# Kernel tuning notes

Measured on AMD Instinct MI355X. Metric: run time of the kernel, lower is better.

## Reference

```python
import jax, jax.numpy as jnp
import numpy as np

N = 100000
E = 1600000
F_IN = 128
HID = 64
HEADS = 2
OUT_HEADS = 1
NUM_CLASS = 18
NEG_SLOPE = 0.2


def setup_inputs() -> dict:
    key = jax.random.key(0)
    ks = jax.random.split(key, 12)
    x = jax.random.normal(ks[0], (N, F_IN), dtype=jnp.float32)
    edge_index = jax.random.randint(ks[1], (2, E), 0, N, dtype=jnp.int64)
    s = lambda k, shp, fan: jax.random.normal(k, shp, dtype=jnp.float32) * (1.0 / np.sqrt(fan))
    W0 = s(ks[2], (F_IN, HID), F_IN)
    b0 = jnp.zeros((HID,), dtype=jnp.float32)
    W1 = s(ks[3], (HID, HEADS * HID), HID)
    att_src1 = s(ks[4], (HEADS, HID), HID)
    att_dst1 = s(ks[5], (HEADS, HID), HID)
    b1 = jnp.zeros((HEADS * HID,), dtype=jnp.float32)
    W2 = s(ks[6], (HEADS * HID, OUT_HEADS * NUM_CLASS), HEADS * HID)
    att_src2 = s(ks[7], (OUT_HEADS, NUM_CLASS), NUM_CLASS)
    att_dst2 = s(ks[8], (OUT_HEADS, NUM_CLASS), NUM_CLASS)
    b2 = jnp.zeros((OUT_HEADS * NUM_CLASS,), dtype=jnp.float32)
    return {"x": x, "edge_index": edge_index, "W0": W0, "b0": b0,
            "W1": W1, "att_src1": att_src1, "att_dst1": att_dst1, "b1": b1,
            "W2": W2, "att_src2": att_src2, "att_dst2": att_dst2, "b2": b2}


def gat_conv(x, src, dst, W, att_s, att_d, bias, heads, out_ch):
    n = x.shape[0]
    h = (x @ W).reshape(n, heads, out_ch)              # [N,H,C]
    a_s = jnp.sum(h * att_s, axis=-1)                   # [N,H]
    a_d = jnp.sum(h * att_d, axis=-1)                   # [N,H]
    e = jax.nn.leaky_relu(a_s[src] + a_d[dst], NEG_SLOPE)  # [E,H]
    m = jax.ops.segment_max(e, dst, num_segments=n)
    ex = jnp.exp(e - m[dst])
    denom = jax.ops.segment_sum(ex, dst, num_segments=n)
    alpha = ex / denom[dst]                              # [E,H]
    msg = h[src] * alpha[:, :, None]                     # [E,H,C]
    out = jax.ops.segment_sum(msg, dst, num_segments=n)  # [N,H,C]
    return out.reshape(n, heads * out_ch) + bias


def reference(x, edge_index, W0, b0, W1, att_src1, att_dst1, b1, W2, att_src2, att_dst2, b2):
    n = x.shape[0]
    # PyG GATConv adds self-loops by default
    loops = jnp.arange(n, dtype=edge_index.dtype)
    src = jnp.concatenate([edge_index[0], loops])
    dst = jnp.concatenate([edge_index[1], loops])
    # eval mode: dropout is identity
    h = jax.nn.relu(x @ W0 + b0)
    h = jax.nn.elu(gat_conv(h, src, dst, W1, att_src1, att_dst1, b1, HEADS, HID))
    out = gat_conv(h, src, dst, W2, att_src2, att_dst2, b2, OUT_HEADS, NUM_CLASS)
    return jax.nn.log_softmax(out, axis=-1)
```

## Files before the change

### kernel.cpp

```cpp
#include <hip/hip_runtime.h>
#include <math.h>


#define NEG_SLOPE 0.2f

typedef unsigned short ushort_t;

__device__ __forceinline__ float wmax(float v) {
    for (int o = 32; o; o >>= 1) v = fmaxf(v, __shfl_xor(v, o));
    return v;
}
__device__ __forceinline__ float wsum(float v) {
    for (int o = 32; o; o >>= 1) v += __shfl_xor(v, o);
    return v;
}

__device__ __forceinline__ unsigned bfpack(float a, float b) {
    unsigned ua = __float_as_uint(a);
    unsigned ub = __float_as_uint(b);
    ua = (ua + 0x7fffu + ((ua >> 16) & 1u)) >> 16;
    ub = (ub + 0x7fffu + ((ub >> 16) & 1u)) & 0xffff0000u;
    return ua | ub;
}
__device__ __forceinline__ ushort_t bf16of(float a) {
    unsigned ua = __float_as_uint(a);
    return (ushort_t)((ua + 0x7fffu + ((ua >> 16) & 1u)) >> 16);
}
__device__ __forceinline__ float bflo(unsigned u) { return __uint_as_float(u << 16); }
__device__ __forceinline__ float bfhi(unsigned u) { return __uint_as_float(u & 0xffff0000u); }
__device__ __forceinline__ float bfval(ushort_t u) { return __uint_as_float(((unsigned)u) << 16); }

__global__ void k_deg_init(int* __restrict__ deg, int N) {
    int i = blockIdx.x * blockDim.x + threadIdx.x;
    if (i < N) deg[i] = 1;
}
__global__ void k_deg_edges(const int* __restrict__ ei, int* __restrict__ deg,
                            int* __restrict__ eofs, int E) {
    int e = blockIdx.x * blockDim.x + threadIdx.x;
    if (e < E) eofs[e] = atomicAdd(&deg[ei[E + e]], 1);
}

__global__ __launch_bounds__(256) void k_scan1(const int* __restrict__ deg, int* __restrict__ rs,
                                               int* __restrict__ bsum, int N) {
    __shared__ int s[256];
    int t = threadIdx.x;
    int base = blockIdx.x * 1024;
    int i0 = base + t * 4;
    int d0 = (i0 + 0 < N) ? deg[i0 + 0] : 0;
    int d1 = (i0 + 1 < N) ? deg[i0 + 1] : 0;
    int d2 = (i0 + 2 < N) ? deg[i0 + 2] : 0;
    int d3 = (i0 + 3 < N) ? deg[i0 + 3] : 0;
    int s0 = d0, s1 = s0 + d1, s2 = s1 + d2, s3 = s2 + d3;
    int tsum = s3;
    s[t] = tsum;
    __syncthreads();
    for (int off = 1; off < 256; off <<= 1) {
        int v = (t >= off) ? s[t - off] : 0;
        __syncthreads();
        s[t] += v;
        __syncthreads();
    }
    int excl = s[t] - tsum;
    if (i0 + 0 < N) rs[1 + i0 + 0] = excl + s0;
    if (i0 + 1 < N) rs[1 + i0 + 1] = excl + s1;
    if (i0 + 2 < N) rs[1 + i0 + 2] = excl + s2;
    if (i0 + 3 < N) rs[1 + i0 + 3] = excl + s3;
    if (t == 0) bsum[blockIdx.x] = s[255];
}

__global__ __launch_bounds__(256) void k_scan2(const int* __restrict__ bsum,
                                               int* __restrict__ boff, int NB) {
    __shared__ int s[256];
    int t = threadIdx.x;
    int orig = (t < NB) ? bsum[t] : 0;
    s[t] = orig;
    __syncthreads();
    for (int off = 1; off < 256; off <<= 1) {
        int v = (t >= off) ? s[t - off] : 0;
        __syncthreads();
        s[t] += v;
        __syncthreads();
    }
    if (t < NB) boff[t] = s[t] - orig;
}

__global__ void k_scan3(int* __restrict__ rs, const int* __restrict__ boff, int N) {
    int i = blockIdx.x * blockDim.x + threadIdx.x;
    if (i == 0) rs[0] = 0;
    if (i < N) rs[1 + i] += boff[i >> 10];
}

__global__ __launch_bounds__(256) void k_scatter(const int* __restrict__ ei,
                                                 const int* __restrict__ eofs,
                                                 const int* __restrict__ rs,
                                                 int* __restrict__ csr,
                                                 int E, int Etot, int cohortBlocks) {
    int c = blockIdx.x & 7;
    int pb = blockIdx.x >> 3;
    int tid = pb * 256 + threadIdx.x;
    int stride = cohortBlocks * 256;
    for (int e = tid; e < Etot; e += stride) {
        int dst = (e < E) ? ei[E + e] : (e - E);
        if (((dst >> 13) & 7) != c) continue;
        int src, ofs;
        if (e < E) { src = ei[e]; ofs = eofs[e]; } else { src = dst; ofs = 0; }
        csr[rs[dst] + ofs] = src;
    }
}


__global__ __launch_bounds__(256) void k_gemm1(const float* __restrict__ x,
                                               const float* __restrict__ W0,
                                               const float* __restrict__ b0,
                                               float* __restrict__ h0, int N) {
    __shared__ float wl[128 * 64];
    __shared__ float al[64 * 132];
    int t = threadIdx.x;
    int n0 = blockIdx.x * 64;
    const float4* wg = (const float4*)W0;
    float4* wl4 = (float4*)wl;
#pragma unroll
    for (int i = 0; i < 8; ++i) wl4[t + i * 256] = wg[t + i * 256];
#pragma unroll
    for (int i = 0; i < 8; ++i) {
        int f = t + i * 256;
        int node = f >> 5, q = f & 31;
        int ng = n0 + node; if (ng > N - 1) ng = N - 1;
        float4 v = ((const float4*)x)[(size_t)ng * 32 + q];
        *(float4*)&al[node * 132 + q * 4] = v;
    }
    __syncthreads();
    int colg = t & 15;
    int rowg = t >> 4;
    float4 acc[4];
#pragma unroll
    for (int j = 0; j < 4; ++j) acc[j] = make_float4(0.f, 0.f, 0.f, 0.f);
    for (int k4 = 0; k4 < 128; k4 += 4) {
        float4 w0 = *(float4*)&wl[(k4 + 0) * 64 + colg * 4];
        float4 w1 = *(float4*)&wl[(k4 + 1) * 64 + colg * 4];
        float4 w2 = *(float4*)&wl[(k4 + 2) * 64 + colg * 4];
        float4 w3 = *(float4*)&wl[(k4 + 3) * 64 + colg * 4];
#pragma unroll
        for (int j = 0; j < 4; ++j) {
            float4 a = *(float4*)&al[(rowg * 4 + j) * 132 + k4];
            acc[j].x += a.x * w0.x + a.y * w1.x + a.z * w2.x + a.w * w3.x;
            acc[j].y += a.x * w0.y + a.y * w1.y + a.z * w2.y + a.w * w3.y;
            acc[j].z += a.x * w0.z + a.y * w1.z + a.z * w2.z + a.w * w3.z;
            acc[j].w += a.x * w0.w + a.y * w1.w + a.z * w2.w + a.w * w3.w;
        }
    }
    float4 bb = ((const float4*)b0)[colg];
#pragma unroll
    for (int j = 0; j < 4; ++j) {
        int n = n0 + rowg * 4 + j;
        if (n < N) {
            float4 r;
            r.x = fmaxf(acc[j].x + bb.x, 0.f);
            r.y = fmaxf(acc[j].y + bb.y, 0.f);
            r.z = fmaxf(acc[j].z + bb.z, 0.f);
            r.w = fmaxf(acc[j].w + bb.w, 0.f);
            ((float4*)h0)[(size_t)n * 16 + colg] = r;
        }
    }
}

__global__ __launch_bounds__(256) void k_gemm2(const float* __restrict__ h0,
                                               const float* __restrict__ W1,
                                               const float* __restrict__ as_g,
                                               const float* __restrict__ ad_g,
                                               ushort_t* __restrict__ h1b,
                                               float* __restrict__ as1,
                                               float* __restrict__ ad1, int N) {
    __shared__ float wl[64 * 128];
    __shared__ float al[64 * 68];
    int t = threadIdx.x;
    int n0 = blockIdx.x * 64;
    const float4* wg = (const float4*)W1;
    float4* wl4 = (float4*)wl;
#pragma unroll
    for (int i = 0; i < 8; ++i) wl4[t + i * 256] = wg[t + i * 256];
#pragma unroll
    for (int i = 0; i < 4; ++i) {
        int f = t + i * 256;
        int node = f >> 4, q = f & 15;
        int ng = n0 + node; if (ng > N - 1) ng = N - 1;
        float4 v = ((const float4*)h0)[(size_t)ng * 16 + q];
        *(float4*)&al[node * 68 + q * 4] = v;
    }
    __syncthreads();
    int colg = t & 31;
    int rowg = t >> 5;
    float4 acc[8];
#pragma unroll
    for (int j = 0; j < 8; ++j) acc[j] = make_float4(0.f, 0.f, 0.f, 0.f);
    for (int k4 = 0; k4 < 64; k4 += 4) {
        float4 w0 = *(float4*)&wl[(k4 + 0) * 128 + colg * 4];
        float4 w1 = *(float4*)&wl[(k4 + 1) * 128 + colg * 4];
        float4 w2 = *(float4*)&wl[(k4 + 2) * 128 + colg * 4];
        float4 w3 = *(float4*)&wl[(k4 + 3) * 128 + colg * 4];
#pragma unroll
        for (int j = 0; j < 8; ++j) {
            float4 a = *(float4*)&al[(rowg * 8 + j) * 68 + k4];
            acc[j].x += a.x * w0.x + a.y * w1.x + a.z * w2.x + a.w * w3.x;
            acc[j].y += a.x * w0.y + a.y * w1.y + a.z * w2.y + a.w * w3.y;
            acc[j].z += a.x * w0.z + a.y * w1.z + a.z * w2.z + a.w * w3.z;
            acc[j].w += a.x * w0.w + a.y * w1.w + a.z * w2.w + a.w * w3.w;
        }
    }
    float4 asv = ((const float4*)as_g)[colg];
    float4 adv = ((const float4*)ad_g)[colg];
    float ps[8], pd[8];
#pragma unroll
    for (int j = 0; j < 8; ++j) {
        ps[j] = acc[j].x * asv.x + acc[j].y * asv.y + acc[j].z * asv.z + acc[j].w * asv.w;
        pd[j] = acc[j].x * adv.x + acc[j].y * adv.y + acc[j].z * adv.z + acc[j].w * adv.w;
    }
    for (int o = 1; o < 16; o <<= 1) {
#pragma unroll
        for (int j = 0; j < 8; ++j) {
            ps[j] += __shfl_xor(ps[j], o);
            pd[j] += __shfl_xor(pd[j], o);
        }
    }
#pragma unroll
    for (int j = 0; j < 8; ++j) {
        int n = n0 + rowg * 8 + j;
        if (n < N) {
            uint2 pr;
            pr.x = bfpack(acc[j].x, acc[j].y);
            pr.y = bfpack(acc[j].z, acc[j].w);
            ((uint2*)h1b)[(size_t)n * 32 + colg] = pr;
        }
    }
    int lane = t & 63;
    if ((lane & 15) == 0) {
        int head = (lane >> 4) & 1;
#pragma unroll
        for (int j = 0; j < 8; ++j) {
            int n = n0 + rowg * 8 + j;
            if (n < N) {
                as1[n * 2 + head] = ps[j];
                ad1[n * 2 + head] = pd[j];
            }
        }
    }
}

__global__ __launch_bounds__(256) void k_node_l1(const int* __restrict__ rs,
                                                 const int* __restrict__ csr,
                                                 const ushort_t* __restrict__ h1b,
                                                 const float* __restrict__ as1,
                                                 const float* __restrict__ ad1,
                                                 const float* __restrict__ b1,
                                                 float* __restrict__ agg, int N) {
    int lane = threadIdx.x & 63;
    int n = (blockIdx.x * 256 + threadIdx.x) >> 6;
    if (n >= N) return;
    int row = rs[n], end = rs[n + 1];
    float2 adv = ((const float2*)ad1)[n];
    const float2* asp = (const float2*)as1;
    const unsigned* h1u = (const unsigned*)h1b;
    bool head1 = lane >= 32;
    float m0 = -INFINITY, m1 = -INFINITY, l0 = 0.f, l1 = 0.f;
    float accx = 0.f, accy = 0.f;
    for (int base = row; base < end; base += 64) {
        int idx = base + lane;
        bool act = idx < end;
        int src = act ? csr[idx] : 0;
        float2 av = asp[src];
        float e0 = av.x + adv.x, e1 = av.y + adv.y;
        e0 = e0 > 0.f ? e0 : NEG_SLOPE * e0;
        e1 = e1 > 0.f ? e1 : NEG_SLOPE * e1;
        if (!act) { e0 = -INFINITY; e1 = -INFINITY; }
        float m0n = fmaxf(m0, wmax(e0));
        float m1n = fmaxf(m1, wmax(e1));
        float r0 = __expf(m0 - m0n), r1 = __expf(m1 - m1n);
        float p0 = act ? __expf(e0 - m0n) : 0.f;
        float p1 = act ? __expf(e1 - m1n) : 0.f;
        l0 = l0 * r0 + wsum(p0);
        l1 = l1 * r1 + wsum(p1);
        float rr = head1 ? r1 : r0;
        accx *= rr; accy *= rr;
        int cnt = min(64, end - base);
#pragma unroll 4
        for (int j = 0; j < cnt; ++j) {
            int sj = __shfl(src, j);
            float a0j = __shfl(p0, j);
            float a1j = __shfl(p1, j);
            float aj = head1 ? a1j : a0j;
            unsigned u = h1u[(size_t)sj * 64 + lane];
            accx += bflo(u) * aj;
            accy += bfhi(u) * aj;
        }
        m0 = m0n; m1 = m1n;
    }
    float inv = 1.f / (head1 ? l1 : l0);
    float vx = accx * inv + b1[lane * 2];
    float vy = accy * inv + b1[lane * 2 + 1];
    vx = vx > 0.f ? vx : expm1f(vx);
    vy = vy > 0.f ? vy : expm1f(vy);
    float2 r; r.x = vx; r.y = vy;
    ((float2*)(agg + (size_t)n * 128))[lane] = r;
}

__global__ __launch_bounds__(256, 4) void k_node2(const float* __restrict__ h1a,
                                                  const float* __restrict__ W2,
                                                  const float* __restrict__ as_g,
                                                  const float* __restrict__ ad_g,
                                                  ushort_t* __restrict__ h2b,
                                                  float* __restrict__ a_s,
                                                  float* __restrict__ a_d, int N) {
    __shared__ float al[64 * 132];
    __shared__ float w2t[20 * 132];
    int t = threadIdx.x;
    int n0 = blockIdx.x * 64;
#pragma unroll
    for (int i = 0; i < 8; ++i) {
        int f = t + i * 256;
        int node = f >> 5, q = f & 31;
        int ng = n0 + node; if (ng > N - 1) ng = N - 1;
        float4 v = ((const float4*)h1a)[(size_t)ng * 32 + q];
        *(float4*)&al[node * 132 + q * 4] = v;
    }
    for (int i = t; i < 2560; i += 256) {
        int c = i >> 7, k = i & 127;
        w2t[c * 132 + k] = (c < 18) ? W2[k * 18 + c] : 0.f;
    }
    __syncthreads();
    int node = t >> 2;
    int cq = t & 3;
    int c0 = cq * 5;
    int n = n0 + node;
    float acc[5] = {0.f, 0.f, 0.f, 0.f, 0.f};
#pragma unroll 2
    for (int k4 = 0; k4 < 128; k4 += 4) {
        float4 a = *(float4*)&al[node * 132 + k4];
#pragma unroll
        for (int i = 0; i < 5; ++i) {
            float4 w = *(float4*)&w2t[(c0 + i) * 132 + k4];
            acc[i] += a.x * w.x + a.y * w.y + a.z * w.z + a.w * w.w;
        }
    }
    float ps = 0.f, pd = 0.f;
#pragma unroll
    for (int i = 0; i < 5; ++i) {
        int c = c0 + i;
        float asv = (c < 18) ? as_g[c] : 0.f;
        float adv = (c < 18) ? ad_g[c] : 0.f;
        ps += acc[i] * asv;
        pd += acc[i] * adv;
    }
    ps += __shfl_xor(ps, 1); ps += __shfl_xor(ps, 2);
    pd += __shfl_xor(pd, 1); pd += __shfl_xor(pd, 2);
    if (n < N) {
#pragma unroll
        for (int i = 0; i < 5; ++i) {
            int c = c0 + i;
            if (c < 18) h2b[(size_t)n * 24 + c] = bf16of(acc[i]);
        }
        if (cq == 0) { a_s[n] = ps; a_d[n] = pd; }
    }
}

__global__ __launch_bounds__(256) void k_node_l2(const int* __restrict__ rs,
                                                 const int* __restrict__ csr,
                                                 const ushort_t* __restrict__ h2b,
                                                 const float* __restrict__ as2,
                                                 const float* __restrict__ ad2,
                                                 const float* __restrict__ b2,
                                                 float* __restrict__ out, int N) {
    int lane = threadIdx.x & 63;
    int n = (blockIdx.x * 256 + threadIdx.x) >> 6;
    if (n >= N) return;
    int row = rs[n], end = rs[n + 1];
    float adn = ad2[n];
    float m = -INFINITY, l = 0.f;
    for (int base = row; base < end; base += 64) {
        int idx = base + lane;
        bool act = idx < end;
        int src = act ? csr[idx] : 0;
        float e = as2[src] + adn;
        e = e > 0.f ? e : NEG_SLOPE * e;
        if (!act) e = -INFINITY;
        float mn = fmaxf(m, wmax(e));
        float p = act ? __expf(e - mn) : 0.f;
        l = l * __expf(m - mn) + wsum(p);
        m = mn;
    }
    float invl = 1.f / l;
    int g = lane / 21;
    int c = lane - g * 21;
    int cc = c < 18 ? c : 17;
    float acc = 0.f;
    for (int pos = row + g; pos < end; pos += 3) {
        int src = csr[pos];
        float e = as2[src] + adn;
        e = e > 0.f ? e : NEG_SLOPE * e;
        float alpha = __expf(e - m) * invl;
        acc += alpha * bfval(h2b[(size_t)src * 24 + cc]);
    }
    float t1 = __shfl(acc, (lane + 21) & 63);
    float t2 = __shfl(acc, (lane + 42) & 63);
    acc += t1 + t2;
    float bb = (lane < 18) ? b2[lane] : 0.f;
    float v = acc + bb;
    float tmx = (lane < 18) ? v : -INFINITY;
    for (int o = 16; o; o >>= 1) tmx = fmaxf(tmx, __shfl_xor(tmx, o));
    float s = (lane < 18) ? __expf(v - tmx) : 0.f;
    for (int o = 16; o; o >>= 1) s += __shfl_xor(s, o);
    float lse = tmx + __logf(s);
    if (lane < 18) out[(size_t)n * 18 + lane] = v - lse;
}

extern "C" void kernel_launch(void* const* d_in, const int* in_sizes, int n_in,
                              void* d_out, int out_size, void* d_ws, size_t ws_size,
                              hipStream_t stream) {
    const float* x      = (const float*)d_in[0];
    const int*   ei     = (const int*)d_in[1];
    const float* W0     = (const float*)d_in[2];
    const float* b0     = (const float*)d_in[3];
    const float* W1     = (const float*)d_in[4];
    const float* att_s1 = (const float*)d_in[5];
    const float* att_d1 = (const float*)d_in[6];
    const float* b1     = (const float*)d_in[7];
    const float* W2     = (const float*)d_in[8];
    const float* att_s2 = (const float*)d_in[9];
    const float* att_d2 = (const float*)d_in[10];
    const float* b2     = (const float*)d_in[11];

    const int N = in_sizes[0] / 128;
    const int E = in_sizes[1] / 2;
    const int Etot = E + N;
    const int NB = (N + 1023) / 1024;
    const int NBLK = (N + 63) / 64;

    char* w = (char*)d_ws;
    float* h0      = (float*)w;    w += (size_t)N * 64 * 4;
    ushort_t* h1b  = (ushort_t*)w; w += (size_t)N * 128 * 2;
    float* agg1    = (float*)w;    w += (size_t)N * 128 * 4;
    float* as1     = (float*)w;    w += (size_t)N * 2 * 4;
    float* ad1     = (float*)w;    w += (size_t)N * 2 * 4;
    ushort_t* h2b  = (ushort_t*)w; w += (size_t)N * 24 * 2;
    float* as2     = (float*)w;    w += (size_t)N * 4;
    float* ad2     = (float*)w;    w += (size_t)N * 4;
    int* deg       = (int*)w;      w += (size_t)N * 4;
    int* rs        = (int*)w;      w += (size_t)(N + 1) * 4;
    int* bsum      = (int*)w;      w += (size_t)256 * 4;
    int* boff      = (int*)w;      w += (size_t)256 * 4;
    int* eofs      = (int*)w;      w += (size_t)E * 4;
    int* csr       = (int*)w;      w += (size_t)Etot * 4;

    float* out = (float*)d_out;

    k_deg_init<<<(N + 255) / 256, 256, 0, stream>>>(deg, N);
    k_deg_edges<<<(E + 255) / 256, 256, 0, stream>>>(ei, deg, eofs, E);
    k_scan1<<<NB, 256, 0, stream>>>(deg, rs, bsum, N);
    k_scan2<<<1, 256, 0, stream>>>(bsum, boff, NB);
    k_scan3<<<(N + 255) / 256, 256, 0, stream>>>(rs, boff, N);
    const int cohortBlocks = 128;
    k_scatter<<<8 * cohortBlocks, 256, 0, stream>>>(ei, eofs, rs, csr, E, Etot, cohortBlocks);

    k_gemm1<<<NBLK, 256, 0, stream>>>(x, W0, b0, h0, N);
    k_gemm2<<<NBLK, 256, 0, stream>>>(h0, W1, att_s1, att_d1, h1b, as1, ad1, N);

    k_node_l1<<<(N * 64 + 255) / 256, 256, 0, stream>>>(rs, csr, h1b, as1, ad1, b1, agg1, N);

    k_node2<<<NBLK, 256, 0, stream>>>(agg1, W2, att_s2, att_d2, h2b, as2, ad2, N);
    k_node_l2<<<(N * 64 + 255) / 256, 256, 0, stream>>>(rs, csr, h2b, as2, ad2, b2, out, N);
}
```

Before: 524.0 us.

## Use two-pass softmax and an LDS broadcast stash in layer-1 aggregation

The layer-1 node kernel replaces its online softmax with two passes. The first pass computes the per-head max and denominator; the second recomputes the normalized attention weights and writes each (src, alpha) pair into a per-wave LDS stash. The inner aggregation loop then reads that pair with one broadcast LDS load instead of three cross-lane shuffles, and the per-chunk accumulator rescaling and final division go away. In exchange, the neighbor indices and source attention scores are gathered a second time, and correctness relies on intra-wave LDS ordering without an explicit barrier.

```diff
diff --git a/kernel.cpp b/kernel.cpp
--- a/kernel.cpp
+++ b/kernel.cpp
@@ -253,6 +253,8 @@
                                                  const float* __restrict__ ad1,
                                                  const float* __restrict__ b1,
                                                  float* __restrict__ agg, int N) {
+    __shared__ float2 stash[4][128];
+    int wid = threadIdx.x >> 6;
     int lane = threadIdx.x & 63;
     int n = (blockIdx.x * 256 + threadIdx.x) >> 6;
     if (n >= N) return;
@@ -260,9 +262,7 @@
     float2 adv = ((const float2*)ad1)[n];
     const float2* asp = (const float2*)as1;
     const unsigned* h1u = (const unsigned*)h1b;
-    bool head1 = lane >= 32;
     float m0 = -INFINITY, m1 = -INFINITY, l0 = 0.f, l1 = 0.f;
-    float accx = 0.f, accy = 0.f;
     for (int base = row; base < end; base += 64) {
         int idx = base + lane;
         bool act = idx < end;
@@ -274,29 +274,41 @@
         if (!act) { e0 = -INFINITY; e1 = -INFINITY; }
         float m0n = fmaxf(m0, wmax(e0));
         float m1n = fmaxf(m1, wmax(e1));
-        float r0 = __expf(m0 - m0n), r1 = __expf(m1 - m1n);
         float p0 = act ? __expf(e0 - m0n) : 0.f;
         float p1 = act ? __expf(e1 - m1n) : 0.f;
-        l0 = l0 * r0 + wsum(p0);
-        l1 = l1 * r1 + wsum(p1);
-        float rr = head1 ? r1 : r0;
-        accx *= rr; accy *= rr;
+        l0 = l0 * __expf(m0 - m0n) + wsum(p0);
+        l1 = l1 * __expf(m1 - m1n) + wsum(p1);
+        m0 = m0n; m1 = m1n;
+    }
+    float inv0 = 1.f / l0, inv1 = 1.f / l1;
+    bool head1 = lane >= 32;
+    float accx = 0.f, accy = 0.f;
+    const float2* sp = &stash[wid][head1 ? 64 : 0];
+    for (int base = row; base < end; base += 64) {
+        int idx = base + lane;
+        bool act = idx < end;
+        int src = act ? csr[idx] : 0;
+        float2 av = asp[src];
+        float e0 = av.x + adv.x, e1 = av.y + adv.y;
+        e0 = e0 > 0.f ? e0 : NEG_SLOPE * e0;
+        e1 = e1 > 0.f ? e1 : NEG_SLOPE * e1;
+        float a0 = act ? __expf(e0 - m0) * inv0 : 0.f;
+        float a1 = act ? __expf(e1 - m1) * inv1 : 0.f;
+        stash[wid][lane] = make_float2(__int_as_float(src), a0);
+        stash[wid][64 + lane] = make_float2(__int_as_float(src), a1);
         int cnt = min(64, end - base);
 #pragma unroll 4
         for (int j = 0; j < cnt; ++j) {
-            int sj = __shfl(src, j);
-            float a0j = __shfl(p0, j);
-            float a1j = __shfl(p1, j);
-            float aj = head1 ? a1j : a0j;
+            float2 sa = sp[j];
+            int sj = __float_as_int(sa.x);
+            float aj = sa.y;
             unsigned u = h1u[(size_t)sj * 64 + lane];
             accx += bflo(u) * aj;
             accy += bfhi(u) * aj;
         }
-        m0 = m0n; m1 = m1n;
-    }
-    float inv = 1.f / (head1 ? l1 : l0);
-    float vx = accx * inv + b1[lane * 2];
-    float vy = accy * inv + b1[lane * 2 + 1];
+    }
+    float vx = accx + b1[lane * 2];
+    float vy = accy + b1[lane * 2 + 1];
     vx = vx > 0.f ? vx : expm1f(vx);
     vy = vy > 0.f ? vy : expm1f(vy);
     float2 r; r.x = vx; r.y = vy;
```

New measurement: 478.2 us. 1.1x faster.
